# Performance work log

Hardware: AMD Instinct MI355X
Metric: run time of the kernel (lower is better)

The kernel has to match this reference:

```python
import jax, jax.numpy as jnp
import numpy as np

N = 100000      # nodes
E = 1600000     # edges (before self loops)
H = 64          # hidden per head (heads=1)
CLASSES = 4
NEG = 0.2       # GATv2 leaky relu slope


def _glorot(key, shape):
    lim = (6.0 / (shape[0] + shape[1])) ** 0.5
    return jax.random.uniform(key, shape, jnp.float32, -lim, lim)


def setup_inputs() -> dict:
    key = jax.random.key(0)
    ks = jax.random.split(key, 40)
    inp = {}
    inp['x'] = jax.random.normal(ks[0], (N, 6), jnp.float32)
    inp['edge_index'] = jax.random.randint(ks[1], (2, E), 0, N, dtype=jnp.int64)
    inp['edge_attr'] = jax.random.normal(ks[2], (E, 6), jnp.float32)
    i = 3
    for l, din in ((1, 6), (2, H), (3, H)):
        inp[f'wl{l}'] = _glorot(ks[i], (din, H)); i += 1
        inp[f'bl{l}'] = jnp.zeros((H,), jnp.float32)
        inp[f'wr{l}'] = _glorot(ks[i], (din, H)); i += 1
        inp[f'br{l}'] = jnp.zeros((H,), jnp.float32)
        inp[f'we{l}'] = _glorot(ks[i], (6, H)); i += 1
        inp[f'att{l}'] = _glorot(ks[i], (H, 1))[:, 0]; i += 1
        inp[f'bo{l}'] = jnp.zeros((H,), jnp.float32)
    inp['wlin'] = _glorot(ks[i], (H, 32)); i += 1
    inp['blin'] = jnp.zeros((32,), jnp.float32)
    inp['wout'] = _glorot(ks[i], (32, CLASSES)); i += 1
    inp['bout'] = jnp.zeros((CLASSES,), jnp.float32)
    return inp


def _add_self_loops(src, dst, ea):
    # PyG add_self_loops(fill_value='mean'): loop attr = mean of incoming edge_attr per node
    cnt = jax.ops.segment_sum(jnp.ones((ea.shape[0],), jnp.float32), dst, num_segments=N)
    loop = jax.ops.segment_sum(ea, dst, num_segments=N) / jnp.maximum(cnt, 1.0)[:, None]
    ar = jnp.arange(N, dtype=src.dtype)
    return (jnp.concatenate([src, ar]), jnp.concatenate([dst, ar]),
            jnp.concatenate([ea, loop], axis=0))


def _gatv2(x, src, dst, ea, wl, bl, wr, br, we, att, bo):
    xl = x @ wl + bl                      # [N,H] source transform
    xr = x @ wr + br                      # [N,H] target transform
    xe = ea @ we                          # [E',H] edge transform (no bias)
    m = xl[src] + xr[dst] + xe            # [E',H]
    e = jax.nn.leaky_relu(m, NEG) @ att   # [E'] attention logits
    emax = jax.ops.segment_max(e, dst, num_segments=N)   # every node has a self loop
    ex = jnp.exp(e - emax[dst])
    den = jax.ops.segment_sum(ex, dst, num_segments=N)
    alpha = ex / (den[dst] + 1e-16)
    out = jax.ops.segment_sum(alpha[:, None] * xl[src], dst, num_segments=N)
    return out + bo


def reference(x, edge_index, edge_attr,
              wl1, bl1, wr1, br1, we1, att1, bo1,
              wl2, bl2, wr2, br2, we2, att2, bo2,
              wl3, bl3, wr3, br3, we3, att3, bo3,
              wlin, blin, wout, bout):
    src, dst, ea = _add_self_loops(edge_index[0], edge_index[1], edge_attr)
    h = jax.nn.relu(_gatv2(x, src, dst, ea, wl1, bl1, wr1, br1, we1, att1, bo1))
    h = jax.nn.relu(_gatv2(h, src, dst, ea, wl2, bl2, wr2, br2, we2, att2, bo2))
    h = jax.nn.relu(_gatv2(h, src, dst, ea, wl3, bl3, wr3, br3, we3, att3, bo3))
    h = jax.nn.relu(h @ wlin + blin)
    return h @ wout + bout
```

## Files before the change

### kernel.cpp

```cpp
#include <hip/hip_runtime.h>
#include <hip/hip_bf16.h>
#include <math.h>

#define NN 100000
#define NE 1600000
#define NEP 1700000
#define HD 64
#define NEGS 0.2f

typedef float f2 __attribute__((ext_vector_type(2)));
typedef float f4 __attribute__((ext_vector_type(4)));

__device__ __forceinline__ f2 sp2(float v) { return (f2){v, v}; }
__device__ __forceinline__ f4 sp4(float v) { return (f4){v, v, v, v}; }
__device__ __forceinline__ f2 ffma2(f2 a, f2 b, f2 c) {
#if __has_builtin(__builtin_elementwise_fma)
  return __builtin_elementwise_fma(a, b, c);
#else
  return a * b + c;
#endif
}
__device__ __forceinline__ f4 ffma4(f4 a, f4 b, f4 c) {
#if __has_builtin(__builtin_elementwise_fma)
  return __builtin_elementwise_fma(a, b, c);
#else
  return a * b + c;
#endif
}
__device__ __forceinline__ f2 fmax2(f2 a, f2 b) {
#if __has_builtin(__builtin_elementwise_max)
  return __builtin_elementwise_max(a, b);
#else
  f2 r; r.x = fmaxf(a.x, b.x); r.y = fmaxf(a.y, b.y); return r;
#endif
}
__device__ __forceinline__ f4 fmax4(f4 a, f4 b) {
#if __has_builtin(__builtin_elementwise_max)
  return __builtin_elementwise_max(a, b);
#else
  f4 r; r.x = fmaxf(a.x, b.x); r.y = fmaxf(a.y, b.y);
  r.z = fmaxf(a.z, b.z); r.w = fmaxf(a.w, b.w); return r;
#endif
}


__global__ void k_init_cnt(int* __restrict__ cnt, int* __restrict__ hist,
                           int* __restrict__ cursor2) {
  int i = blockIdx.x * 256 + threadIdx.x;
  if (i < NN) cnt[i] = 1;
  if (blockIdx.x == 0) {
    if (threadIdx.x < 64) hist[threadIdx.x] = 0;
    else if (threadIdx.x < 128) cursor2[threadIdx.x - 64] = 0;
  }
}

__global__ void k_count_rank(const int* __restrict__ dst, int* __restrict__ cnt,
                             int* __restrict__ rank) {
  int base = (blockIdx.x * 256 + threadIdx.x) * 4;
  if (base >= NE) return;
  int4 dv = *(const int4*)(dst + base);
  int4 rv;
  rv.x = atomicAdd(&cnt[dv.x], 1);
  rv.y = atomicAdd(&cnt[dv.y], 1);
  rv.z = atomicAdd(&cnt[dv.z], 1);
  rv.w = atomicAdd(&cnt[dv.w], 1);
  *(int4*)(rank + base) = rv;
}

__global__ void k_scan_a(const int* __restrict__ cnt, int* __restrict__ rp,
                         int* __restrict__ bsum, int* __restrict__ hist) {
  __shared__ int tmp[1024];
  __shared__ int lh[64];
  int t = threadIdx.x, b = blockIdx.x;
  int i = b * 1024 + t;
  int v = (i < NN) ? cnt[i] : 0;
  tmp[t] = v;
  if (t < 64) lh[t] = 0;
  __syncthreads();
  if (i < NN) atomicAdd(&lh[v < 63 ? v : 63], 1);
  for (int off = 1; off < 1024; off <<= 1) {
    int a = (t >= off) ? tmp[t - off] : 0;
    __syncthreads(); tmp[t] += a; __syncthreads();
  }
  if (i < NN) rp[i] = tmp[t] - v;
  if (t == 1023) bsum[b] = tmp[t];
  if (t < 64) { int h = lh[t]; if (h) atomicAdd(&hist[t], h); }
}

__global__ void k_scan_b(const int* __restrict__ bsum, int* __restrict__ boff, int nb,
                         const int* __restrict__ hist, int* __restrict__ cursor2) {
  __shared__ int tmp[1024];
  int t = threadIdx.x;
  int v = (t < nb) ? bsum[t] : 0;
  tmp[t] = v; __syncthreads();
  for (int off = 1; off < 1024; off <<= 1) {
    int a = (t >= off) ? tmp[t - off] : 0;
    __syncthreads(); tmp[t] += a; __syncthreads();
  }
  if (t < nb) boff[t] = tmp[t] - v;
  if (t < 64) {
    int h = hist[t];
    int s = h;
#pragma unroll
    for (int off = 1; off < 64; off <<= 1) {
      int u = __shfl_up(s, off);
      if (t >= off) s += u;
    }
    cursor2[t] = s - h;
  }
}

__global__ void k_scan_c(int* __restrict__ rp, const int* __restrict__ boff,
                         const int* __restrict__ deg,
                         int* __restrict__ cursor2, int* __restrict__ order) {
  __shared__ int lh[64];
  __shared__ int lbase[64];
  int t = threadIdx.x, b = blockIdx.x;
  int i = b * 1024 + t;
  if (t < 64) lh[t] = 0;
  __syncthreads();
  int bin = 0, lr = 0;
  if (i < NN) {
    int d = deg[i];
    bin = d < 63 ? d : 63;
    lr = atomicAdd(&lh[bin], 1);
    rp[i] = rp[i] + boff[b];
  }
  __syncthreads();
  if (t < 64) {
    int h = lh[t];
    lbase[t] = h ? atomicAdd(&cursor2[t], h) : 0;
  }
  __syncthreads();
  if (i < NN) order[lbase[bin] + lr] = i;
  if (i == 0) rp[NN] = NEP;
}

__global__ void __launch_bounds__(256) k_scatter3(
    const int* __restrict__ src, const int* __restrict__ dst,
    const int* __restrict__ rank, const float* __restrict__ ea,
    const int* __restrict__ rp, float* __restrict__ rec) {
  int base = (blockIdx.x * 256 + threadIdx.x) * 4;
  if (base >= NE) return;
  int4 sv = *(const int4*)(src + base);
  int4 dv = *(const int4*)(dst + base);
  int4 rv = *(const int4*)(rank + base);
  const float4* e4 = (const float4*)(ea + (size_t)base * 6);
  float4 e0 = e4[0], e1 = e4[1], e2 = e4[2], e3 = e4[3], e4v = e4[4], e5 = e4[5];
  int d[4] = {dv.x, dv.y, dv.z, dv.w};
  int rk[4] = {rv.x, rv.y, rv.z, rv.w};
  int s[4] = {sv.x, sv.y, sv.z, sv.w};
  int p[4];
#pragma unroll
  for (int k = 0; k < 4; ++k) p[k] = rp[d[k]] + rk[k];
  float a[24] = {e0.x, e0.y, e0.z, e0.w, e1.x, e1.y, e1.z, e1.w,
                 e2.x, e2.y, e2.z, e2.w, e3.x, e3.y, e3.z, e3.w,
                 e4v.x, e4v.y, e4v.z, e4v.w, e5.x, e5.y, e5.z, e5.w};
#pragma unroll
  for (int k = 0; k < 4; ++k) {
    float* r = rec + (size_t)p[k] * 8;
    *(float4*)r       = make_float4(__int_as_float(s[k]),
                                    a[6 * k + 0], a[6 * k + 1], a[6 * k + 2]);
    *(float4*)(r + 4) = make_float4(a[6 * k + 3], a[6 * k + 4], a[6 * k + 5], 0.f);
  }
}

__global__ void __launch_bounds__(256) k_lamean2(const int* __restrict__ rp,
                                                 float* __restrict__ rec) {
  int tid = threadIdx.x;
  int q = tid & 15;
  int n = (blockIdx.x * 256 + tid) >> 4;
  if (n >= NN) return;
  int p0 = rp[n], p1 = rp[n + 1];
  float s0 = 0, s1 = 0, s2 = 0, s3 = 0, s4 = 0, s5 = 0;
  for (int p = p0 + 1 + q; p < p1; p += 16) {
    const float* r = rec + (size_t)p * 8;
    float4 r0 = *(const float4*)r;
    float4 r1 = *(const float4*)(r + 4);
    s0 += r0.y; s1 += r0.z; s2 += r0.w;
    s3 += r1.x; s4 += r1.y; s5 += r1.z;
  }
#pragma unroll
  for (int off = 1; off < 16; off <<= 1) {
    s0 += __shfl_xor(s0, off); s1 += __shfl_xor(s1, off);
    s2 += __shfl_xor(s2, off); s3 += __shfl_xor(s3, off);
    s4 += __shfl_xor(s4, off); s5 += __shfl_xor(s5, off);
  }
  if (q == 0) {
    int c = p1 - p0 - 1;
    float inv = c > 0 ? 1.0f / (float)c : 0.0f;
    float* r = rec + (size_t)p0 * 8;
    *(float4*)r       = make_float4(__int_as_float(n), s0 * inv, s1 * inv, s2 * inv);
    *(float4*)(r + 4) = make_float4(s3 * inv, s4 * inv, s5 * inv, 0.f);
  }
}

template <int DIN>
__global__ void __launch_bounds__(256) k_xform(
    const float* __restrict__ x,
    const float* __restrict__ wl, const float* __restrict__ bl,
    const float* __restrict__ wr, const float* __restrict__ br,
    float* __restrict__ xl, float* __restrict__ xr) {
  __shared__ f2 wpk_s[DIN * 64];
  int tid = threadIdx.x;
  int lane = tid & 63, wid = tid >> 6;
  int h = lane;
  for (int idx = tid; idx < DIN * 64; idx += 256)
    wpk_s[idx] = (f2){wl[idx], wr[idx]};
  __syncthreads();
  f2 bpk = (f2){bl[h], br[h]};
  int gw = blockIdx.x * 4 + wid;
  int nw = gridDim.x * 4;
  const int NG = NN / 4;
  for (int g = gw; g < NG; g += nw) {
    int n0 = g * 4;
    float xv[4];
#pragma unroll
    for (int j = 0; j < 4; ++j)
      xv[j] = (lane < DIN) ? x[(size_t)(n0 + j) * DIN + lane] : 0.0f;
    f2 acc[4];
#pragma unroll
    for (int j = 0; j < 4; ++j) acc[j] = bpk;
#pragma unroll
    for (int k = 0; k < DIN; ++k) {
      f2 w = wpk_s[k * 64 + h];
#pragma unroll
      for (int j = 0; j < 4; ++j) {
        float xk = __shfl(xv[j], k);
        acc[j] = ffma2(sp2(xk), w, acc[j]);
      }
    }
#pragma unroll
    for (int j = 0; j < 4; ++j) {
      xl[(size_t)(n0 + j) * 64 + h] = acc[j].x;
      xr[(size_t)(n0 + j) * 64 + h] = acc[j].y;
    }
  }
}

__global__ void __launch_bounds__(256) k_fused(
    const float* __restrict__ xl, const float* __restrict__ xr,
    const float* __restrict__ rec,
    const int* __restrict__ rp, const int* __restrict__ order,
    const float* __restrict__ we, const float* __restrict__ att,
    const float* __restrict__ bo, float* __restrict__ hout) {
  int tid = threadIdx.x;
  int lane = tid & 63;
  int q = lane & 15;
  int c0 = q * 4;
  f2 w0a, w0b, w1a, w1b, w2a, w2b, w3a, w3b, w4a, w4b, w5a, w5b;
  w0a = *(const f2*)(we + 0 * 64 + c0); w0b = *(const f2*)(we + 0 * 64 + c0 + 2);
  w1a = *(const f2*)(we + 1 * 64 + c0); w1b = *(const f2*)(we + 1 * 64 + c0 + 2);
  w2a = *(const f2*)(we + 2 * 64 + c0); w2b = *(const f2*)(we + 2 * 64 + c0 + 2);
  w3a = *(const f2*)(we + 3 * 64 + c0); w3b = *(const f2*)(we + 3 * 64 + c0 + 2);
  w4a = *(const f2*)(we + 4 * 64 + c0); w4b = *(const f2*)(we + 4 * 64 + c0 + 2);
  w5a = *(const f2*)(we + 5 * 64 + c0); w5b = *(const f2*)(we + 5 * 64 + c0 + 2);
  f2 ata = *(const f2*)(att + c0) * 1.44269504f;
  f2 atb = *(const f2*)(att + c0 + 2) * 1.44269504f;
  f2 boa = *(const f2*)(bo + c0);
  f2 bob = *(const f2*)(bo + c0 + 2);
  int gw = (blockIdx.x * 256 + tid) >> 6;
  int slot = gw * 4 + (lane >> 4);
  int n = (slot < NN) ? order[NN - 1 - slot] : -1;
  int p0 = 0, p1 = 0;
  f2 xra = (f2){0, 0}, xrb2 = (f2){0, 0};
  if (n >= 0) {
    p0 = rp[n]; p1 = rp[n + 1];
    const f4 t = *(const f4*)(xr + (size_t)n * 64 + c0);
    xra = (f2){t.x, t.y}; xrb2 = (f2){t.z, t.w};
  }
  float m = -INFINITY, den = 0.0f;
  f2 acca = (f2){0, 0}, accb = (f2){0, 0};
  int p = p0;
  for (; p + 2 <= p1; p += 2) {
    const f4* ra = (const f4*)(rec + (size_t)p * 8);
    f4 qa0 = ra[0], qa1 = ra[1], qb0 = ra[2], qb1 = ra[3];
    int sA = __float_as_int(qa0.x), sB = __float_as_int(qb0.x);
    f4 xA = *(const f4*)(xl + (size_t)sA * 64 + c0);
    f4 xB = *(const f4*)(xl + (size_t)sB * 64 + c0);
    f2 xAa = (f2){xA.x, xA.y}, xAb = (f2){xA.z, xA.w};
    f2 xBa = (f2){xB.x, xB.y}, xBb = (f2){xB.z, xB.w};
    f2 tA = xAa + xra;
    tA = ffma2(sp2(qa0.y), w0a, tA); tA = ffma2(sp2(qa0.z), w1a, tA);
    tA = ffma2(sp2(qa0.w), w2a, tA); tA = ffma2(sp2(qa1.x), w3a, tA);
    tA = ffma2(sp2(qa1.y), w4a, tA); tA = ffma2(sp2(qa1.z), w5a, tA);
    f2 pav = fmax2(tA, sp2(0.2f) * tA) * ata;
    f2 uA = xAb + xrb2;
    uA = ffma2(sp2(qa0.y), w0b, uA); uA = ffma2(sp2(qa0.z), w1b, uA);
    uA = ffma2(sp2(qa0.w), w2b, uA); uA = ffma2(sp2(qa1.x), w3b, uA);
    uA = ffma2(sp2(qa1.y), w4b, uA); uA = ffma2(sp2(qa1.z), w5b, uA);
    pav = ffma2(fmax2(uA, sp2(0.2f) * uA), atb, pav);
    f2 tB = xBa + xra;
    tB = ffma2(sp2(qb0.y), w0a, tB); tB = ffma2(sp2(qb0.z), w1a, tB);
    tB = ffma2(sp2(qb0.w), w2a, tB); tB = ffma2(sp2(qb1.x), w3a, tB);
    tB = ffma2(sp2(qb1.y), w4a, tB); tB = ffma2(sp2(qb1.z), w5a, tB);
    f2 pbv = fmax2(tB, sp2(0.2f) * tB) * ata;
    f2 uB = xBb + xrb2;
    uB = ffma2(sp2(qb0.y), w0b, uB); uB = ffma2(sp2(qb0.z), w1b, uB);
    uB = ffma2(sp2(qb0.w), w2b, uB); uB = ffma2(sp2(qb1.x), w3b, uB);
    uB = ffma2(sp2(qb1.y), w4b, uB); uB = ffma2(sp2(qb1.z), w5b, uB);
    pbv = ffma2(fmax2(uB, sp2(0.2f) * uB), atb, pbv);
    float pa = pav.x + pav.y;
    float pb = pbv.x + pbv.y;
    pa += __shfl_xor(pa, 1); pb += __shfl_xor(pb, 1);
    pa += __shfl_xor(pa, 2); pb += __shfl_xor(pb, 2);
    pa += __shfl_xor(pa, 4); pb += __shfl_xor(pb, 4);
    pa += __shfl_xor(pa, 8); pb += __shfl_xor(pb, 8);
    float nm = fmaxf(m, fmaxf(pa, pb));
    float sc = exp2f(m - nm);
    float eA = exp2f(pa - nm);
    float eB = exp2f(pb - nm);
    m = nm;
    den = fmaf(den, sc, eA + eB);
    acca = ffma2(acca, sp2(sc), ffma2(sp2(eA), xAa, sp2(eB) * xBa));
    accb = ffma2(accb, sp2(sc), ffma2(sp2(eA), xAb, sp2(eB) * xBb));
  }
  if (p < p1) {
    const f4* ra = (const f4*)(rec + (size_t)p * 8);
    f4 r0 = ra[0], r1 = ra[1];
    int s = __float_as_int(r0.x);
    f4 xt = *(const f4*)(xl + (size_t)s * 64 + c0);
    f2 xa = (f2){xt.x, xt.y}, xb = (f2){xt.z, xt.w};
    f2 t = xa + xra;
    t = ffma2(sp2(r0.y), w0a, t); t = ffma2(sp2(r0.z), w1a, t);
    t = ffma2(sp2(r0.w), w2a, t); t = ffma2(sp2(r1.x), w3a, t);
    t = ffma2(sp2(r1.y), w4a, t); t = ffma2(sp2(r1.z), w5a, t);
    f2 pv = fmax2(t, sp2(0.2f) * t) * ata;
    f2 u = xb + xrb2;
    u = ffma2(sp2(r0.y), w0b, u); u = ffma2(sp2(r0.z), w1b, u);
    u = ffma2(sp2(r0.w), w2b, u); u = ffma2(sp2(r1.x), w3b, u);
    u = ffma2(sp2(r1.y), w4b, u); u = ffma2(sp2(r1.z), w5b, u);
    pv = ffma2(fmax2(u, sp2(0.2f) * u), atb, pv);
    float part = pv.x + pv.y;
    part += __shfl_xor(part, 1);
    part += __shfl_xor(part, 2);
    part += __shfl_xor(part, 4);
    part += __shfl_xor(part, 8);
    float nm = fmaxf(m, part);
    float sc = exp2f(m - nm);
    float ex = exp2f(part - nm);
    m = nm;
    den = fmaf(den, sc, ex);
    acca = ffma2(acca, sp2(sc), sp2(ex) * xa);
    accb = ffma2(accb, sp2(sc), sp2(ex) * xb);
  }
  if (n >= 0) {
    float inv = 1.0f / (den + 1e-16f);
    f2 oa = ffma2(acca, sp2(inv), boa);
    f2 ob = ffma2(accb, sp2(inv), bob);
    oa = fmax2(oa, (f2){0, 0});
    ob = fmax2(ob, (f2){0, 0});
    f4 o = (f4){oa.x, oa.y, ob.x, ob.y};
    *(f4*)(hout + (size_t)n * 64 + c0) = o;
  }
}

__global__ void __launch_bounds__(256) k_mlp2(
    const float* __restrict__ hin,
    const float* __restrict__ wlin, const float* __restrict__ blin,
    const float* __restrict__ wout, const float* __restrict__ bout,
    float* __restrict__ out) {
  __shared__ float wl_s[64 * 32];
  __shared__ float bl_s[32];
  __shared__ float wo_s[32 * 4];
  __shared__ float bo_s[4];
  int tid = threadIdx.x;
#pragma unroll
  for (int i = 0; i < 8; ++i) wl_s[tid + i * 256] = wlin[tid + i * 256];
  if (tid < 128) wo_s[tid] = wout[tid];
  if (tid < 32) bl_s[tid] = blin[tid];
  if (tid >= 32 && tid < 36) bo_s[tid - 32] = bout[tid - 32];
  __syncthreads();
  int n = blockIdx.x * 256 + tid;
  if (n >= NN) return;
  const f4* hp = (const f4*)(hin + (size_t)n * 64);
  f4 h[16];
#pragma unroll
  for (int i = 0; i < 16; ++i) h[i] = hp[i];
  f4 acc[8];
#pragma unroll
  for (int j4 = 0; j4 < 8; ++j4) acc[j4] = *(const f4*)(bl_s + j4 * 4);
#pragma unroll
  for (int k = 0; k < 64; ++k) {
    float hk = ((const float*)h)[k];
    const f4* wrow = (const f4*)(wl_s + k * 32);
#pragma unroll
    for (int j4 = 0; j4 < 8; ++j4)
      acc[j4] = ffma4(sp4(hk), wrow[j4], acc[j4]);
  }
  f4 o4 = *(const f4*)(bo_s);
#pragma unroll
  for (int j4 = 0; j4 < 8; ++j4) {
    f4 hid = fmax4(acc[j4], sp4(0.0f));
    const f4* wo = (const f4*)(wo_s + j4 * 16);
    o4 = ffma4(sp4(hid.x), wo[0], o4);
    o4 = ffma4(sp4(hid.y), wo[1], o4);
    o4 = ffma4(sp4(hid.z), wo[2], o4);
    o4 = ffma4(sp4(hid.w), wo[3], o4);
  }
  *(f4*)(out + (size_t)n * 4) = o4;
}


extern "C" void kernel_launch(void* const* d_in, const int* in_sizes, int n_in,
                              void* d_out, int out_size, void* d_ws, size_t ws_size,
                              hipStream_t stream) {
  const float* x  = (const float*)d_in[0];
  const int*   ei = (const int*)d_in[1];
  const float* ea = (const float*)d_in[2];
  const int* src = ei;
  const int* dst = ei + NE;

  const float *wl[3], *bl[3], *wrm[3], *br[3], *wem[3], *attv[3], *bov[3];
  for (int l = 0; l < 3; ++l) {
    int b = 3 + l * 7;
    wl[l]  = (const float*)d_in[b + 0];
    bl[l]  = (const float*)d_in[b + 1];
    wrm[l] = (const float*)d_in[b + 2];
    br[l]  = (const float*)d_in[b + 3];
    wem[l] = (const float*)d_in[b + 4];
    attv[l]= (const float*)d_in[b + 5];
    bov[l] = (const float*)d_in[b + 6];
  }
  const float* wlin = (const float*)d_in[24];
  const float* blin = (const float*)d_in[25];
  const float* wout = (const float*)d_in[26];
  const float* bout = (const float*)d_in[27];
  float* outp = (float*)d_out;

  char* w = (char*)d_ws;
  size_t off = 0;
  auto carve = [&](size_t bytes) -> void* {
    void* p = w + off;
    off += (bytes + 255) & ~(size_t)255;
    return p;
  };
  int*   cnt  = (int*)carve((size_t)NN * 4);
  int*   rp   = (int*)carve((size_t)(NN + 1) * 4);
  int*   bsum = (int*)carve(1024 * 4);
  int*   boff = (int*)carve(1024 * 4);
  int*   hist = (int*)carve(64 * 4);
  int*   cur2 = (int*)carve(64 * 4);
  int*   order= (int*)carve((size_t)NN * 4);
  int*   rank = (int*)carve((size_t)NE * 4);
  float* rec  = (float*)carve((size_t)NEP * 32);
  float* xlb  = (float*)carve((size_t)NN * 64 * 4);
  float* xrb  = (float*)carve((size_t)NN * 64 * 4);
  float* hA   = (float*)carve((size_t)NN * 64 * 4);
  float* hB   = (float*)carve((size_t)NN * 64 * 4);
  (void)ws_size; (void)n_in; (void)in_sizes; (void)out_size;

  const int SCAN_NB = (NN + 1023) / 1024;
  const int FUSE_NB = (NN + 15) / 16;
  const int CR_NB   = (NE / 4 + 255) / 256;
  const int XF_NB   = 1024;

  hipLaunchKernelGGL(k_init_cnt, dim3((NN + 255) / 256), dim3(256), 0, stream,
                     cnt, hist, cur2);
  hipLaunchKernelGGL(k_count_rank, dim3(CR_NB), dim3(256), 0, stream, dst, cnt, rank);
  hipLaunchKernelGGL(k_scan_a, dim3(SCAN_NB), dim3(1024), 0, stream, cnt, rp, bsum, hist);
  hipLaunchKernelGGL(k_scan_b, dim3(1), dim3(1024), 0, stream, bsum, boff, SCAN_NB,
                     hist, cur2);
  hipLaunchKernelGGL(k_scan_c, dim3(SCAN_NB), dim3(1024), 0, stream, rp, boff, cnt,
                     cur2, order);
  hipLaunchKernelGGL(k_scatter3, dim3(CR_NB), dim3(256), 0, stream,
                     src, dst, rank, ea, rp, rec);
  hipLaunchKernelGGL(k_lamean2, dim3((NN + 15) / 16), dim3(256), 0, stream, rp, rec);

  hipLaunchKernelGGL((k_xform<6>), dim3(XF_NB), dim3(256), 0, stream,
                     x, wl[0], bl[0], wrm[0], br[0], xlb, xrb);
  hipLaunchKernelGGL(k_fused, dim3(FUSE_NB), dim3(256), 0, stream,
                     xlb, xrb, rec, rp, order, wem[0], attv[0], bov[0], hA);
  hipLaunchKernelGGL((k_xform<64>), dim3(XF_NB), dim3(256), 0, stream,
                     hA, wl[1], bl[1], wrm[1], br[1], xlb, xrb);
  hipLaunchKernelGGL(k_fused, dim3(FUSE_NB), dim3(256), 0, stream,
                     xlb, xrb, rec, rp, order, wem[1], attv[1], bov[1], hB);
  hipLaunchKernelGGL((k_xform<64>), dim3(XF_NB), dim3(256), 0, stream,
                     hB, wl[2], bl[2], wrm[2], br[2], xlb, xrb);
  hipLaunchKernelGGL(k_fused, dim3(FUSE_NB), dim3(256), 0, stream,
                     xlb, xrb, rec, rp, order, wem[2], attv[2], bov[2], hA);
  hipLaunchKernelGGL(k_mlp2, dim3((NN + 255) / 256), dim3(256), 0, stream,
                     hA, wlin, blin, wout, bout, outp);
}
```

Baseline: 538.1 us.

## Scatter edge ids then sort per node and gather records; widen xform tiles

The 32-byte record scatter is split into two steps. The first scatters only 4-byte edge ids into CSR slots. A per-node wave then bitonic-sorts those ids, so neighbour order is deterministic and matches the original edge order, and gathers src and edge attributes into the records with coalesced writes. The node transform now gives each wave a fixed 8 nodes with no grid-stride loop, using NN/32 blocks. This adds an extra kernel, an eid buffer and random reads of edge attributes. Nodes with more than 64 neighbours fall back to a serial insertion sort on one lane.

```diff
diff --git a/kernel.cpp b/kernel.cpp
--- a/kernel.cpp
+++ b/kernel.cpp
@@ -136,32 +136,71 @@
   if (i == 0) rp[NN] = NEP;
 }
 
-__global__ void __launch_bounds__(256) k_scatter3(
-    const int* __restrict__ src, const int* __restrict__ dst,
-    const int* __restrict__ rank, const float* __restrict__ ea,
-    const int* __restrict__ rp, float* __restrict__ rec) {
+__global__ void __launch_bounds__(256) k_scatter_id(
+    const int* __restrict__ dst, const int* __restrict__ rank,
+    const int* __restrict__ rp, int* __restrict__ eid) {
   int base = (blockIdx.x * 256 + threadIdx.x) * 4;
   if (base >= NE) return;
-  int4 sv = *(const int4*)(src + base);
   int4 dv = *(const int4*)(dst + base);
   int4 rv = *(const int4*)(rank + base);
-  const float4* e4 = (const float4*)(ea + (size_t)base * 6);
-  float4 e0 = e4[0], e1 = e4[1], e2 = e4[2], e3 = e4[3], e4v = e4[4], e5 = e4[5];
-  int d[4] = {dv.x, dv.y, dv.z, dv.w};
-  int rk[4] = {rv.x, rv.y, rv.z, rv.w};
-  int s[4] = {sv.x, sv.y, sv.z, sv.w};
-  int p[4];
-#pragma unroll
-  for (int k = 0; k < 4; ++k) p[k] = rp[d[k]] + rk[k];
-  float a[24] = {e0.x, e0.y, e0.z, e0.w, e1.x, e1.y, e1.z, e1.w,
-                 e2.x, e2.y, e2.z, e2.w, e3.x, e3.y, e3.z, e3.w,
-                 e4v.x, e4v.y, e4v.z, e4v.w, e5.x, e5.y, e5.z, e5.w};
-#pragma unroll
-  for (int k = 0; k < 4; ++k) {
-    float* r = rec + (size_t)p[k] * 8;
-    *(float4*)r       = make_float4(__int_as_float(s[k]),
-                                    a[6 * k + 0], a[6 * k + 1], a[6 * k + 2]);
-    *(float4*)(r + 4) = make_float4(a[6 * k + 3], a[6 * k + 4], a[6 * k + 5], 0.f);
+  eid[rp[dv.x] + rv.x] = base + 0;
+  eid[rp[dv.y] + rv.y] = base + 1;
+  eid[rp[dv.z] + rv.z] = base + 2;
+  eid[rp[dv.w] + rv.w] = base + 3;
+}
+
+__global__ void __launch_bounds__(256) k_sortscat(
+    const int* __restrict__ rp, int* __restrict__ eid,
+    const int* __restrict__ src, const float* __restrict__ ea,
+    float* __restrict__ rec) {
+  int tid = threadIdx.x;
+  int lane = tid & 63, wid = tid >> 6;
+  int n = blockIdx.x * 4 + wid;
+  if (n >= NN) return;
+  int p0 = rp[n], p1 = rp[n + 1];
+  int len = p1 - p0 - 1;
+  if (len <= 0) return;
+  if (len <= 64) {
+    int v = (lane < len) ? eid[p0 + 1 + lane] : 0x7fffffff;
+#pragma unroll
+    for (int k = 2; k <= 64; k <<= 1) {
+#pragma unroll
+      for (int j = k >> 1; j > 0; j >>= 1) {
+        int u = __shfl_xor(v, j);
+        bool up = ((lane & k) == 0);
+        bool lower = ((lane & j) == 0);
+        int mn = v < u ? v : u;
+        int mx = v < u ? u : v;
+        v = (up == lower) ? mn : mx;
+      }
+    }
+    if (lane < len) {
+      int id = v;
+      f2 e01 = *(const f2*)(ea + (size_t)id * 6);
+      f2 e23 = *(const f2*)(ea + (size_t)id * 6 + 2);
+      f2 e45 = *(const f2*)(ea + (size_t)id * 6 + 4);
+      int s = src[id];
+      float* r = rec + (size_t)(p0 + 1 + lane) * 8;
+      *(f4*)r       = (f4){__int_as_float(s), e01.x, e01.y, e23.x};
+      *(f4*)(r + 4) = (f4){e23.y, e45.x, e45.y, 0.f};
+    }
+  } else {
+    if (lane == 0) {
+      for (int a = p0 + 2; a < p1; ++a) {
+        int key = eid[a], b = a - 1;
+        while (b > p0 && eid[b] > key) { eid[b + 1] = eid[b]; --b; }
+        eid[b + 1] = key;
+      }
+      for (int p = p0 + 1; p < p1; ++p) {
+        int id = eid[p];
+        f2 e01 = *(const f2*)(ea + (size_t)id * 6);
+        f2 e23 = *(const f2*)(ea + (size_t)id * 6 + 2);
+        f2 e45 = *(const f2*)(ea + (size_t)id * 6 + 4);
+        float* r = rec + (size_t)p * 8;
+        *(f4*)r       = (f4){__int_as_float(src[id]), e01.x, e01.y, e23.x};
+        *(f4*)(r + 4) = (f4){e23.y, e45.x, e45.y, 0.f};
+      }
+    }
   }
 }
 
@@ -196,45 +235,40 @@
 }
 
 template <int DIN>
-__global__ void __launch_bounds__(256) k_xform(
+__global__ void __launch_bounds__(256) k_xform4(
     const float* __restrict__ x,
     const float* __restrict__ wl, const float* __restrict__ bl,
     const float* __restrict__ wr, const float* __restrict__ br,
     float* __restrict__ xl, float* __restrict__ xr) {
-  __shared__ f2 wpk_s[DIN * 64];
+  __shared__ f2 w_s[DIN * 64];
   int tid = threadIdx.x;
+  for (int idx = tid; idx < DIN * 64; idx += 256)
+    w_s[idx] = (f2){wl[idx], wr[idx]};
+  __syncthreads();
   int lane = tid & 63, wid = tid >> 6;
   int h = lane;
-  for (int idx = tid; idx < DIN * 64; idx += 256)
-    wpk_s[idx] = (f2){wl[idx], wr[idx]};
-  __syncthreads();
   f2 bpk = (f2){bl[h], br[h]};
-  int gw = blockIdx.x * 4 + wid;
-  int nw = gridDim.x * 4;
-  const int NG = NN / 4;
-  for (int g = gw; g < NG; g += nw) {
-    int n0 = g * 4;
-    float xv[4];
-#pragma unroll
-    for (int j = 0; j < 4; ++j)
-      xv[j] = (lane < DIN) ? x[(size_t)(n0 + j) * DIN + lane] : 0.0f;
-    f2 acc[4];
-#pragma unroll
-    for (int j = 0; j < 4; ++j) acc[j] = bpk;
-#pragma unroll
-    for (int k = 0; k < DIN; ++k) {
-      f2 w = wpk_s[k * 64 + h];
-#pragma unroll
-      for (int j = 0; j < 4; ++j) {
-        float xk = __shfl(xv[j], k);
-        acc[j] = ffma2(sp2(xk), w, acc[j]);
-      }
+  int n0 = (blockIdx.x * 4 + wid) * 8;
+  float xv[8];
+#pragma unroll
+  for (int j = 0; j < 8; ++j)
+    xv[j] = (lane < DIN) ? x[(size_t)(n0 + j) * DIN + lane] : 0.0f;
+  f2 acc[8];
+#pragma unroll
+  for (int j = 0; j < 8; ++j) acc[j] = bpk;
+#pragma unroll
+  for (int k = 0; k < DIN; ++k) {
+    f2 w = w_s[k * 64 + h];
+#pragma unroll
+    for (int j = 0; j < 8; ++j) {
+      float xk = __shfl(xv[j], k);
+      acc[j] = ffma2(sp2(xk), w, acc[j]);
     }
-#pragma unroll
-    for (int j = 0; j < 4; ++j) {
-      xl[(size_t)(n0 + j) * 64 + h] = acc[j].x;
-      xr[(size_t)(n0 + j) * 64 + h] = acc[j].y;
-    }
+  }
+#pragma unroll
+  for (int j = 0; j < 8; ++j) {
+    xl[(size_t)(n0 + j) * 64 + h] = acc[j].x;
+    xr[(size_t)(n0 + j) * 64 + h] = acc[j].y;
   }
 }
 
@@ -443,6 +477,7 @@
   int*   cur2 = (int*)carve(64 * 4);
   int*   order= (int*)carve((size_t)NN * 4);
   int*   rank = (int*)carve((size_t)NE * 4);
+  int*   eid  = (int*)carve((size_t)NEP * 4);
   float* rec  = (float*)carve((size_t)NEP * 32);
   float* xlb  = (float*)carve((size_t)NN * 64 * 4);
   float* xrb  = (float*)carve((size_t)NN * 64 * 4);
@@ -453,7 +488,8 @@
   const int SCAN_NB = (NN + 1023) / 1024;
   const int FUSE_NB = (NN + 15) / 16;
   const int CR_NB   = (NE / 4 + 255) / 256;
-  const int XF_NB   = 1024;
+  const int XF_NB   = NN / 32;
+  const int SS_NB   = (NN + 3) / 4;
 
   hipLaunchKernelGGL(k_init_cnt, dim3((NN + 255) / 256), dim3(256), 0, stream,
                      cnt, hist, cur2);
@@ -463,19 +499,21 @@
                      hist, cur2);
   hipLaunchKernelGGL(k_scan_c, dim3(SCAN_NB), dim3(1024), 0, stream, rp, boff, cnt,
                      cur2, order);
-  hipLaunchKernelGGL(k_scatter3, dim3(CR_NB), dim3(256), 0, stream,
-                     src, dst, rank, ea, rp, rec);
+  hipLaunchKernelGGL(k_scatter_id, dim3(CR_NB), dim3(256), 0, stream,
+                     dst, rank, rp, eid);
+  hipLaunchKernelGGL(k_sortscat, dim3(SS_NB), dim3(256), 0, stream,
+                     rp, eid, src, ea, rec);
   hipLaunchKernelGGL(k_lamean2, dim3((NN + 15) / 16), dim3(256), 0, stream, rp, rec);
 
-  hipLaunchKernelGGL((k_xform<6>), dim3(XF_NB), dim3(256), 0, stream,
+  hipLaunchKernelGGL((k_xform4<6>), dim3(XF_NB), dim3(256), 0, stream,
                      x, wl[0], bl[0], wrm[0], br[0], xlb, xrb);
   hipLaunchKernelGGL(k_fused, dim3(FUSE_NB), dim3(256), 0, stream,
                      xlb, xrb, rec, rp, order, wem[0], attv[0], bov[0], hA);
-  hipLaunchKernelGGL((k_xform<64>), dim3(XF_NB), dim3(256), 0, stream,
+  hipLaunchKernelGGL((k_xform4<64>), dim3(XF_NB), dim3(256), 0, stream,
                      hA, wl[1], bl[1], wrm[1], br[1], xlb, xrb);
   hipLaunchKernelGGL(k_fused, dim3(FUSE_NB), dim3(256), 0, stream,
                      xlb, xrb, rec, rp, order, wem[1], attv[1], bov[1], hB);
-  hipLaunchKernelGGL((k_xform<64>), dim3(XF_NB), dim3(256), 0, stream,
+  hipLaunchKernelGGL((k_xform4<64>), dim3(XF_NB), dim3(256), 0, stream,
                      hB, wl[2], bl[2], wrm[2], br[2], xlb, xrb);
   hipLaunchKernelGGL(k_fused, dim3(FUSE_NB), dim3(256), 0, stream,
                      xlb, xrb, rec, rp, order, wem[2], attv[2], bov[2], hA);
```

Measured after the change: 605.8 us. +12.6%, slower.
